# Kernel optimization log

Hardware: AMD Instinct MI355X
Metric: run time of the kernel (lower is better)

## Reference

```python
import jax, jax.numpy as jnp
import numpy as np

BITS = 4
GROUP_SIZE = 128
INF, OUTF, TOKENS = 4096, 11008, 256


def setup_inputs() -> dict:
    key = jax.random.key(0)
    k1, k2, k3, k4, k5 = jax.random.split(key, 5)
    n_groups = INF // GROUP_SIZE  # 32
    x = jax.random.normal(k1, (TOKENS, INF), dtype=jnp.float32)
    qweight = jax.random.randint(k2, (INF // 32 * BITS, OUTF), 0, 2**31 - 1, dtype=jnp.int32)
    qzeros = jax.random.randint(k3, (n_groups, OUTF // 32 * BITS), 0, 2**31 - 1, dtype=jnp.int32)
    scales = jax.random.uniform(k4, (n_groups, OUTF), dtype=jnp.float32, minval=1e-3, maxval=2e-2)
    bias = jax.random.normal(k5, (OUTF,), dtype=jnp.float32)
    return {"x": x, "qweight": qweight, "qzeros": qzeros, "scales": scales, "bias": bias}


def _dequantize(qweight, qzeros, scales):
    """Unpack int4 nibbles and build the fp32 weight [infeatures, outfeatures]."""
    shifts = jnp.arange(0, 32, BITS, dtype=jnp.int32)  # [8]
    mask = (1 << BITS) - 1
    out_f = qweight.shape[1]
    # qweight row packs 8 consecutive in-features -> [K, O] int in [0, 15]
    w = ((qweight[:, None, :] >> shifts[None, :, None]) & mask).reshape(-1, out_f)
    # qzeros col packs 8 consecutive out-features; stored as (zero - 1)
    n_groups = qzeros.shape[0]
    z = (((qzeros[:, :, None] >> shifts[None, None, :]) & mask) + 1).reshape(n_groups, out_f)
    g_idx = jnp.arange(w.shape[0], dtype=jnp.int32) // GROUP_SIZE  # [K]
    return (w - z[g_idx]).astype(jnp.float32) * scales[g_idx]


def reference(x, qweight, qzeros, scales, bias):
    W = _dequantize(qweight, qzeros, scales)  # [infeatures, outfeatures]
    return x @ W + bias  # [tokens, outfeatures]
```

## Files before the change

### kernel.cpp

```cpp
#include <hip/hip_runtime.h>
#include <stdint.h>

#define TOKENS  256
#define INF     4096
#define OUTF    11008
#define NGROUPS 32
#define KSPLIT  2
#define PHK     128
#define NPH     ((INF / KSPLIT) / PHK)
#define NTH     256

typedef __attribute__((ext_vector_type(2))) _Float16 f16x2;
typedef __attribute__((ext_vector_type(8))) _Float16 f16x8;
typedef __attribute__((ext_vector_type(2))) __fp16   pkh2;
typedef __attribute__((ext_vector_type(4))) float    f32x4;

union U32H2 { uint32_t u; f16x2 h; };
union H8    { f16x2 h2[4]; f16x8 h8; };
union PK    { pkh2 p; f16x2 h; };

__device__ __forceinline__ void gl2lds16(const void* g, void* l) {
    __builtin_amdgcn_global_load_lds(
        (const __attribute__((address_space(1))) uint32_t*)g,
        (__attribute__((address_space(3))) uint32_t*)l, 16, 0, 0);
}

__global__ __launch_bounds__(NTH)
void prep(const float* __restrict__ x, _Float16* __restrict__ x16,
          const float* __restrict__ bias, float* __restrict__ out) {
    const int b = blockIdx.x;
    if (b < 512) {
        const int t   = b * NTH + threadIdx.x;
        const int row = t >> 9;
        const int c   = t & 511;
        const float* p = x + (size_t)row * INF + c * 8;
        f32x4 v0 = *(const f32x4*)p;
        f32x4 v1 = *(const f32x4*)(p + 4);
        H8 o; PK k0, k1, k2, k3;
        k0.p = __builtin_amdgcn_cvt_pkrtz(v0[0], v1[0]);
        k1.p = __builtin_amdgcn_cvt_pkrtz(v0[1], v1[1]);
        k2.p = __builtin_amdgcn_cvt_pkrtz(v0[2], v1[2]);
        k3.p = __builtin_amdgcn_cvt_pkrtz(v0[3], v1[3]);
        o.h2[0] = k0.h; o.h2[1] = k1.h; o.h2[2] = k2.h; o.h2[3] = k3.h;
        *(f16x8*)(x16 + (size_t)row * INF + c * 8) = o.h8;
    } else {
        const int t = (b - 512) * NTH + threadIdx.x;
        const int c = t % (OUTF / 4);
        const int r = t / (OUTF / 4);
        const f32x4 bv = ((const f32x4*)bias)[c];
        ((f32x4*)out)[(size_t)r * (OUTF / 4) + c] = bv;
    }
}

__global__ __launch_bounds__(NTH, 3)
void qlin_main(const _Float16* __restrict__ x16,
               const uint32_t* __restrict__ qweight,
               const uint32_t* __restrict__ qzeros,
               const float* __restrict__ scales,
               float* __restrict__ out)
{
    __shared__ alignas(16) _Float16 As[2][64 * PHK];

    const int tid = threadIdx.x;

    const int d  = blockIdx.x;
    const int cx = d & 7, kk = d >> 3;
    int strip, memb;
    if (kk < 80) { strip = cx * 10 + (kk >> 3); memb = kk & 7; }
    else         { const int t2 = ((kk - 80) << 3) | cx; strip = 80 + (t2 >> 3); memb = t2 & 7; }
    const int bx = strip;
    const int by = memb >> 1;
    const int ks = memb & 1;

    const int lane = tid & 63;
    const int quad = lane >> 4;
    const int l16  = lane & 15;
    const int wv   = tid >> 6;

    const int rowoff = tid >> 4;
    const int chk    = tid & 15;
    const int row0   = by * 64;
    const uint32_t aoff = (uint32_t)((row0 + rowoff) * (INF * 2)
                                     + ks * (INF / KSPLIT) * 2
                                     + ((chk ^ rowoff) & 15) * 16);
    const char* x16b = (const char*)x16;
    _Float16* ldsW = &As[0][0];
    const int ldsSlotBase = wv * 512;

    const int col0 = bx * 128 + wv * 32 + l16;
    const int col1 = col0 + 16;
    const int bOff0 = quad * OUTF + col0;
    const int bOff1 = quad * OUTF + col1;
    const int zsh   = (col0 & 7) * 4;
    const int qrow0 = ks * (INF / KSPLIT / 8);
    const int g0    = ks * (NGROUPS / KSPLIT);

    f32x4 acc[4][2];
#pragma unroll
    for (int mi = 0; mi < 4; ++mi)
#pragma unroll
        for (int nf = 0; nf < 2; ++nf)
            acc[mi][nf] = f32x4{0.f, 0.f, 0.f, 0.f};

    uint32_t Breg[2][8];
    float    sS[2][2];
    uint32_t qZ[2][2];

#pragma unroll
    for (int r = 0; r < 4; ++r)
        gl2lds16(x16b + aoff + r * 131072, ldsW + r * 2048 + ldsSlotBase);
    __builtin_amdgcn_sched_barrier(0);
    {
        sS[0][0] = scales[g0 * OUTF + col0];
        sS[0][1] = scales[g0 * OUTF + col1];
        qZ[0][0] = qzeros[g0 * (OUTF / 8) + (col0 >> 3)];
        qZ[0][1] = qzeros[g0 * (OUTF / 8) + (col1 >> 3)];
        const uint32_t* qp = qweight + (size_t)qrow0 * OUTF;
#pragma unroll
        for (int s = 0; s < 4; ++s) {
            Breg[0][2 * s + 0] = qp[(size_t)(s * 4) * OUTF + bOff0];
            Breg[0][2 * s + 1] = qp[(size_t)(s * 4) * OUTF + bOff1];
        }
    }

#define PHASE_BODY(PAR, P, DO_PREFETCH)                                          \
    {                                                                            \
        __builtin_amdgcn_sched_barrier(0);                                       \
        asm volatile("s_waitcnt vmcnt(8)" ::: "memory");                         \
        __builtin_amdgcn_s_barrier();                                            \
        __builtin_amdgcn_sched_barrier(0);                                       \
        if (DO_PREFETCH) {                                                       \
            const int pn = (P) + 1;                                              \
            const uint32_t pb = (uint32_t)(pn * (PHK * 2));                      \
            _Float16* ldsN = ldsW + (1 - (PAR)) * 8192;                          \
            _Pragma("unroll")                                                    \
            for (int r = 0; r < 4; ++r)                                          \
                gl2lds16(x16b + aoff + r * 131072 + pb,                          \
                         ldsN + r * 2048 + ldsSlotBase);                         \
            __builtin_amdgcn_sched_barrier(0);           \
            const int gn = g0 + pn;                                              \
            sS[1 - (PAR)][0] = scales[gn * OUTF + col0];                         \
            sS[1 - (PAR)][1] = scales[gn * OUTF + col1];                         \
            qZ[1 - (PAR)][0] = qzeros[gn * (OUTF / 8) + (col0 >> 3)];            \
            qZ[1 - (PAR)][1] = qzeros[gn * (OUTF / 8) + (col1 >> 3)];            \
            const uint32_t* qpb = qweight + (size_t)(qrow0 + pn * 16) * OUTF;    \
            _Pragma("unroll")                                                    \
            for (int s = 0; s < 4; ++s) {                                        \
                Breg[1 - (PAR)][2 * s + 0] = qpb[(size_t)(s * 4) * OUTF + bOff0];\
                Breg[1 - (PAR)][2 * s + 1] = qpb[(size_t)(s * 4) * OUTF + bOff1];\
            }                                                                    \
        }                                                                        \
        f16x2 hs2[2], hz2[2];                                                    \
        _Pragma("unroll")                                                        \
        for (int nf = 0; nf < 2; ++nf) {                                         \
            const float s = sS[PAR][nf];                                         \
            const int   z = (int)((qZ[PAR][nf] >> zsh) & 15u) + 1025;            \
            const _Float16 hs = (_Float16)s;                                     \
            const _Float16 hz = (_Float16)(-(float)z);                           \
            hs2[nf] = f16x2{hs, hs};                                             \
            hz2[nf] = f16x2{hz, hz};                                             \
        }                                                                        \
        const _Float16* buf = ldsW + (PAR) * 8192;                               \
        _Pragma("unroll")                                                        \
        for (int s = 0; s < 4; ++s) {                                            \
            f16x8 af[4];                                                         \
            _Pragma("unroll")                                                    \
            for (int mi = 0; mi < 4; ++mi) {                                     \
                const int m  = mi * 16 + l16;                                    \
                const int sc = ((s * 4 + quad) ^ l16) & 15;                      \
                af[mi] = *(const f16x8*)(buf + m * PHK + sc * 8);                \
            }                                                                    \
            _Pragma("unroll")                                                    \
            for (int nf = 0; nf < 2; ++nf) {                                     \
                const uint32_t q = Breg[PAR][2 * s + nf];                        \
                H8 b;                                                            \
                _Pragma("unroll")                                                \
                for (int j = 0; j < 4; ++j) {                                    \
                    U32H2 u;                                                     \
                    u.u = ((q >> (4 * j)) & 0x000F000Fu) | 0x64006400u;          \
                    b.h2[j] = (u.h + hz2[nf]) * hs2[nf];                         \
                }                                                                \
                __builtin_amdgcn_s_setprio(1);                                   \
                _Pragma("unroll")                                                \
                for (int mi = 0; mi < 4; ++mi)                                   \
                    acc[mi][nf] = __builtin_amdgcn_mfma_f32_16x16x32_f16(        \
                        af[mi], b.h8, acc[mi][nf], 0, 0, 0);                     \
                __builtin_amdgcn_s_setprio(0);                                   \
            }                                                                    \
        }                                                                        \
    }

#pragma unroll 1
    for (int pp = 0; pp < NPH / 2; ++pp) {
        PHASE_BODY(0, 2 * pp, true)
        PHASE_BODY(1, 2 * pp + 1, (pp < NPH / 2 - 1))
    }
#undef PHASE_BODY

#pragma unroll
    for (int nf = 0; nf < 2; ++nf) {
        const int col = (nf == 0) ? col0 : col1;
#pragma unroll
        for (int mi = 0; mi < 4; ++mi) {
            const int r0 = by * 64 + mi * 16 + quad * 4;
#pragma unroll
            for (int rg = 0; rg < 4; ++rg)
                unsafeAtomicAdd(&out[(size_t)(r0 + rg) * OUTF + col],
                                acc[mi][nf][rg]);
        }
    }
}

__global__ __launch_bounds__(NTH, 2)
void qlin_fb(const float* __restrict__ x,
             const uint32_t* __restrict__ qweight,
             const uint32_t* __restrict__ qzeros,
             const float* __restrict__ scales,
             const float* __restrict__ bias,
             float* __restrict__ out)
{
    __shared__ alignas(16) _Float16 Asb[64][40];
    __shared__ alignas(16) _Float16 Bsb[128][40];
    const int tid = threadIdx.x;
    const int bx = blockIdx.x, by = blockIdx.y;
    const int am = tid >> 2, ar = tid & 3;
    const float* xrow = x + (size_t)(by * 64 + am) * INF + ar * 8;
    const int bc = tid & 127, br = tid >> 7;
    const int bn = bx * 128 + bc;
    const int bswz = (bc >> 3) & 3;
    const int lane = tid & 63, quad = lane >> 4, l16 = lane & 15;
    const int wv = tid >> 6, wm = wv >> 1, wn = wv & 1;
    f32x4 acc[2][4];
#pragma unroll
    for (int i = 0; i < 2; ++i)
#pragma unroll
        for (int j = 0; j < 4; ++j) acc[i][j] = f32x4{0.f, 0.f, 0.f, 0.f};
    f32x4 pa0 = *(const f32x4*)(xrow + 0);
    f32x4 pa1 = *(const f32x4*)(xrow + 4);
    uint32_t pq0 = qweight[(size_t)br * OUTF + bn];
    uint32_t pq1 = qweight[(size_t)(br + 2) * OUTF + bn];
    for (int g = 0; g < NGROUPS; ++g) {
        const float s = scales[g * OUTF + bn];
        const uint32_t qzv = qzeros[g * (OUTF / 8) + (bn >> 3)];
        const int z = (int)((qzv >> (4 * (bn & 7))) & 15u) + 1;
        const _Float16 hs = (_Float16)s;
        const _Float16 hz = (_Float16)(-(float)(1024 + z));
        const f16x2 hs2 = {hs, hs}, hz2 = {hz, hz};
#pragma unroll
        for (int t4 = 0; t4 < 4; ++t4) {
            const int it = (g << 2) + t4;
            { H8 ah; PK p0, p1, p2, p3;
              p0.p = __builtin_amdgcn_cvt_pkrtz(pa0[0], pa1[0]);
              p1.p = __builtin_amdgcn_cvt_pkrtz(pa0[1], pa1[1]);
              p2.p = __builtin_amdgcn_cvt_pkrtz(pa0[2], pa1[2]);
              p3.p = __builtin_amdgcn_cvt_pkrtz(pa0[3], pa1[3]);
              ah.h2[0] = p0.h; ah.h2[1] = p1.h; ah.h2[2] = p2.h; ah.h2[3] = p3.h;
              *(f16x8*)&Asb[am][ar * 8] = ah.h8; }
            { const uint32_t qq[2] = {pq0, pq1};
#pragma unroll
              for (int rr = 0; rr < 2; ++rr) {
                  const int r = br + rr * 2; H8 bh;
#pragma unroll
                  for (int jp = 0; jp < 4; ++jp) {
                      U32H2 u; u.u = ((qq[rr] >> (4 * jp)) & 0x000F000Fu) | 0x64006400u;
                      bh.h2[jp] = (u.h + hz2) * hs2;
                  }
                  *(f16x8*)&Bsb[bc][(r ^ bswz) * 8] = bh.h8;
              } }
            __syncthreads();
            const int itn = (it < 127) ? it + 1 : 127;
            pa0 = *(const f32x4*)(xrow + itn * 32);
            pa1 = *(const f32x4*)(xrow + itn * 32 + 4);
            pq0 = qweight[(size_t)(itn * 4 + br) * OUTF + bn];
            pq1 = qweight[(size_t)(itn * 4 + br + 2) * OUTF + bn];
            f16x8 af[2], bf[4];
#pragma unroll
            for (int mi = 0; mi < 2; ++mi)
                af[mi] = *(const f16x8*)&Asb[wm * 32 + mi * 16 + l16][quad * 8];
#pragma unroll
            for (int ni = 0; ni < 4; ++ni) {
                const int c = wn * 64 + ni * 16 + l16;
                bf[ni] = *(const f16x8*)&Bsb[c][(quad ^ ((c >> 3) & 3)) * 8];
            }
#pragma unroll
            for (int mi = 0; mi < 2; ++mi)
#pragma unroll
                for (int ni = 0; ni < 4; ++ni)
                    acc[mi][ni] = __builtin_amdgcn_mfma_f32_16x16x32_f16(
                        af[mi], bf[ni], acc[mi][ni], 0, 0, 0);
            __syncthreads();
        }
    }
#pragma unroll
    for (int ni = 0; ni < 4; ++ni) {
        const int col = bx * 128 + wn * 64 + ni * 16 + l16;
        const float bv = bias[col];
#pragma unroll
        for (int mi = 0; mi < 2; ++mi) {
            const int row0 = by * 64 + wm * 32 + mi * 16 + quad * 4;
#pragma unroll
            for (int rg = 0; rg < 4; ++rg)
                out[(size_t)(row0 + rg) * OUTF + col] = acc[mi][ni][rg] + bv;
        }
    }
}

extern "C" void kernel_launch(void* const* d_in, const int* in_sizes, int n_in,
                              void* d_out, int out_size, void* d_ws, size_t ws_size,
                              hipStream_t stream) {
    const float*    xx = (const float*)d_in[0];
    const uint32_t* qw = (const uint32_t*)d_in[1];
    const uint32_t* qz = (const uint32_t*)d_in[2];
    const float*    sc = (const float*)d_in[3];
    const float*    bs = (const float*)d_in[4];
    float* out = (float*)d_out;

    const size_t x16_bytes = (size_t)TOKENS * INF * sizeof(_Float16);
    if (ws_size >= x16_bytes) {
        _Float16* x16 = (_Float16*)d_ws;
        prep<<<512 + (TOKENS * OUTF / 4) / NTH, NTH, 0, stream>>>(xx, x16, bs, out);
        qlin_main<<<(OUTF / 128) * (TOKENS / 64) * KSPLIT, NTH, 0, stream>>>(
            x16, qw, qz, sc, out);
    } else {
        dim3 grid(OUTF / 128, TOKENS / 64);
        qlin_fb<<<grid, NTH, 0, stream>>>(xx, qw, qz, sc, bs, out);
    }
}
```

Baseline: 122.2 us.

## Load activation fragments directly from global memory instead of LDS staging

Removes the LDS double buffer for the fp16 activations, along with the global_load_lds prefetch, the vmcnt wait and the block-wide barrier in each phase. Each wave now reads its A fragments straight from global memory (through the cache) just before the MFMAs. This drops the barrier synchronisation and the LDS traffic, but the four waves now each fetch the same A tile redundantly, and those loads are no longer prefetched a phase ahead, so their latency is exposed.

```diff
diff --git a/kernel.cpp b/kernel.cpp
--- a/kernel.cpp
+++ b/kernel.cpp
@@ -18,12 +18,6 @@
 union U32H2 { uint32_t u; f16x2 h; };
 union H8    { f16x2 h2[4]; f16x8 h8; };
 union PK    { pkh2 p; f16x2 h; };
-
-__device__ __forceinline__ void gl2lds16(const void* g, void* l) {
-    __builtin_amdgcn_global_load_lds(
-        (const __attribute__((address_space(1))) uint32_t*)g,
-        (__attribute__((address_space(3))) uint32_t*)l, 16, 0, 0);
-}
 
 __global__ __launch_bounds__(NTH)
 void prep(const float* __restrict__ x, _Float16* __restrict__ x16,
@@ -59,8 +53,6 @@
                const float* __restrict__ scales,
                float* __restrict__ out)
 {
-    __shared__ alignas(16) _Float16 As[2][64 * PHK];
-
     const int tid = threadIdx.x;
 
     const int d  = blockIdx.x;
@@ -77,15 +69,8 @@
     const int l16  = lane & 15;
     const int wv   = tid >> 6;
 
-    const int rowoff = tid >> 4;
-    const int chk    = tid & 15;
-    const int row0   = by * 64;
-    const uint32_t aoff = (uint32_t)((row0 + rowoff) * (INF * 2)
-                                     + ks * (INF / KSPLIT) * 2
-                                     + ((chk ^ rowoff) & 15) * 16);
-    const char* x16b = (const char*)x16;
-    _Float16* ldsW = &As[0][0];
-    const int ldsSlotBase = wv * 512;
+    const _Float16* aBase = x16 + (size_t)(by * 64 + l16) * INF
+                                + ks * (INF / KSPLIT) + quad * 8;
 
     const int col0 = bx * 128 + wv * 32 + l16;
     const int col1 = col0 + 16;
@@ -106,10 +91,6 @@
     float    sS[2][2];
     uint32_t qZ[2][2];
 
-#pragma unroll
-    for (int r = 0; r < 4; ++r)
-        gl2lds16(x16b + aoff + r * 131072, ldsW + r * 2048 + ldsSlotBase);
-    __builtin_amdgcn_sched_barrier(0);
     {
         sS[0][0] = scales[g0 * OUTF + col0];
         sS[0][1] = scales[g0 * OUTF + col1];
@@ -125,19 +106,8 @@
 
 #define PHASE_BODY(PAR, P, DO_PREFETCH)                                          \
     {                                                                            \
-        __builtin_amdgcn_sched_barrier(0);                                       \
-        asm volatile("s_waitcnt vmcnt(8)" ::: "memory");                         \
-        __builtin_amdgcn_s_barrier();                                            \
-        __builtin_amdgcn_sched_barrier(0);                                       \
         if (DO_PREFETCH) {                                                       \
             const int pn = (P) + 1;                                              \
-            const uint32_t pb = (uint32_t)(pn * (PHK * 2));                      \
-            _Float16* ldsN = ldsW + (1 - (PAR)) * 8192;                          \
-            _Pragma("unroll")                                                    \
-            for (int r = 0; r < 4; ++r)                                          \
-                gl2lds16(x16b + aoff + r * 131072 + pb,                          \
-                         ldsN + r * 2048 + ldsSlotBase);                         \
-            __builtin_amdgcn_sched_barrier(0);           \
             const int gn = g0 + pn;                                              \
             sS[1 - (PAR)][0] = scales[gn * OUTF + col0];                         \
             sS[1 - (PAR)][1] = scales[gn * OUTF + col1];                         \
@@ -160,16 +130,13 @@
             hs2[nf] = f16x2{hs, hs};                                             \
             hz2[nf] = f16x2{hz, hz};                                             \
         }                                                                        \
-        const _Float16* buf = ldsW + (PAR) * 8192;                               \
+        const _Float16* aP = aBase + (P) * PHK;                                  \
         _Pragma("unroll")                                                        \
         for (int s = 0; s < 4; ++s) {                                            \
             f16x8 af[4];                                                         \
             _Pragma("unroll")                                                    \
-            for (int mi = 0; mi < 4; ++mi) {                                     \
-                const int m  = mi * 16 + l16;                                    \
-                const int sc = ((s * 4 + quad) ^ l16) & 15;                      \
-                af[mi] = *(const f16x8*)(buf + m * PHK + sc * 8);                \
-            }                                                                    \
+            for (int mi = 0; mi < 4; ++mi)                                       \
+                af[mi] = *(const f16x8*)(aP + (size_t)mi * (16 * INF) + s * 32); \
             _Pragma("unroll")                                                    \
             for (int nf = 0; nf < 2; ++nf) {                                     \
                 const uint32_t q = Breg[PAR][2 * s + nf];                        \
```

New measurement: 173.7 us. 1.42x slower.

## Widen output tile to 256 columns per block to double A-tile reuse

Applied to the files above, without the earlier changes.

Each block now covers 256 output columns, with each wave holding 4 N-fragments, so every A tile staged in LDS feeds twice as many MFMAs. The grid halves to 344 blocks and the block-to-tile mapping is changed to a simple strided interleave. Occupancy drops to 2 blocks per CU because the accumulator and prefetched weight registers double, and the vmcnt wait is raised to match the larger number of in-flight weight loads. The trade is more reuse and less staging of A through LDS, against fewer resident waves and only 344 blocks to spread across the CUs.

```diff
diff --git a/kernel.cpp b/kernel.cpp
--- a/kernel.cpp
+++ b/kernel.cpp
@@ -9,6 +9,7 @@
 #define PHK     128
 #define NPH     ((INF / KSPLIT) / PHK)
 #define NTH     256
+#define BN      256
 
 typedef __attribute__((ext_vector_type(2))) _Float16 f16x2;
 typedef __attribute__((ext_vector_type(8))) _Float16 f16x8;
@@ -52,7 +53,7 @@
     }
 }
 
-__global__ __launch_bounds__(NTH, 3)
+__global__ __launch_bounds__(NTH, 2)
 void qlin_main(const _Float16* __restrict__ x16,
                const uint32_t* __restrict__ qweight,
                const uint32_t* __restrict__ qzeros,
@@ -63,12 +64,10 @@
 
     const int tid = threadIdx.x;
 
-    const int d  = blockIdx.x;
-    const int cx = d & 7, kk = d >> 3;
-    int strip, memb;
-    if (kk < 80) { strip = cx * 10 + (kk >> 3); memb = kk & 7; }
-    else         { const int t2 = ((kk - 80) << 3) | cx; strip = 80 + (t2 >> 3); memb = t2 & 7; }
-    const int bx = strip;
+    const int d   = blockIdx.x;
+    const int lin = (d & 7) * 43 + (d >> 3);
+    const int bx   = lin >> 3;
+    const int memb = lin & 7;
     const int by = memb >> 1;
     const int ks = memb & 1;
 
@@ -87,72 +86,70 @@
     _Float16* ldsW = &As[0][0];
     const int ldsSlotBase = wv * 512;
 
-    const int col0 = bx * 128 + wv * 32 + l16;
-    const int col1 = col0 + 16;
-    const int bOff0 = quad * OUTF + col0;
-    const int bOff1 = quad * OUTF + col1;
-    const int zsh   = (col0 & 7) * 4;
+    int colN[4], bOffN[4], zOffN[4];
+#pragma unroll
+    for (int nf = 0; nf < 4; ++nf) {
+        colN[nf]  = bx * BN + wv * 64 + nf * 16 + l16;
+        bOffN[nf] = quad * OUTF + colN[nf];
+        zOffN[nf] = colN[nf] >> 3;
+    }
+    const int zsh   = (l16 & 7) * 4;
     const int qrow0 = ks * (INF / KSPLIT / 8);
     const int g0    = ks * (NGROUPS / KSPLIT);
 
-    f32x4 acc[4][2];
+    f32x4 acc[4][4];
 #pragma unroll
     for (int mi = 0; mi < 4; ++mi)
 #pragma unroll
-        for (int nf = 0; nf < 2; ++nf)
+        for (int nf = 0; nf < 4; ++nf)
             acc[mi][nf] = f32x4{0.f, 0.f, 0.f, 0.f};
 
-    uint32_t Breg[2][8];
-    float    sS[2][2];
-    uint32_t qZ[2][2];
+    uint32_t Breg[2][16];
+    float    sS[2][4];
+    uint32_t qZ[2][4];
+
+#define LOAD_B(SLOT, PN)                                                         \
+    {                                                                            \
+        const int gn_ = g0 + (PN);                                               \
+        _Pragma("unroll")                                                        \
+        for (int nf = 0; nf < 4; ++nf) {                                         \
+            sS[SLOT][nf] = scales[gn_ * OUTF + colN[nf]];                        \
+            qZ[SLOT][nf] = qzeros[gn_ * (OUTF / 8) + zOffN[nf]];                 \
+        }                                                                        \
+        const uint32_t* qpb_ = qweight + (size_t)(qrow0 + (PN) * 16) * OUTF;     \
+        _Pragma("unroll")                                                        \
+        for (int s_ = 0; s_ < 4; ++s_)                                           \
+            _Pragma("unroll")                                                    \
+            for (int nf = 0; nf < 4; ++nf)                                       \
+                Breg[SLOT][s_ * 4 + nf] =                                        \
+                    qpb_[(size_t)(s_ * 4) * OUTF + bOffN[nf]];                   \
+    }
 
 #pragma unroll
     for (int r = 0; r < 4; ++r)
         gl2lds16(x16b + aoff + r * 131072, ldsW + r * 2048 + ldsSlotBase);
     __builtin_amdgcn_sched_barrier(0);
-    {
-        sS[0][0] = scales[g0 * OUTF + col0];
-        sS[0][1] = scales[g0 * OUTF + col1];
-        qZ[0][0] = qzeros[g0 * (OUTF / 8) + (col0 >> 3)];
-        qZ[0][1] = qzeros[g0 * (OUTF / 8) + (col1 >> 3)];
-        const uint32_t* qp = qweight + (size_t)qrow0 * OUTF;
-#pragma unroll
-        for (int s = 0; s < 4; ++s) {
-            Breg[0][2 * s + 0] = qp[(size_t)(s * 4) * OUTF + bOff0];
-            Breg[0][2 * s + 1] = qp[(size_t)(s * 4) * OUTF + bOff1];
-        }
-    }
-
-#define PHASE_BODY(PAR, P, DO_PREFETCH)                                          \
+    LOAD_B(0, 0)
+
+#define PHASE_BODY(PAR, P, DO_PRE)                                               \
     {                                                                            \
         __builtin_amdgcn_sched_barrier(0);                                       \
-        asm volatile("s_waitcnt vmcnt(8)" ::: "memory");                         \
+        asm volatile("s_waitcnt vmcnt(16)" ::: "memory");                        \
         __builtin_amdgcn_s_barrier();                                            \
         __builtin_amdgcn_sched_barrier(0);                                       \
-        if (DO_PREFETCH) {                                                       \
-            const int pn = (P) + 1;                                              \
-            const uint32_t pb = (uint32_t)(pn * (PHK * 2));                      \
+        if (DO_PRE) {                                                            \
+            const uint32_t pb = (uint32_t)(((P) + 1) * (PHK * 2));               \
             _Float16* ldsN = ldsW + (1 - (PAR)) * 8192;                          \
             _Pragma("unroll")                                                    \
             for (int r = 0; r < 4; ++r)                                          \
                 gl2lds16(x16b + aoff + r * 131072 + pb,                          \
                          ldsN + r * 2048 + ldsSlotBase);                         \
-            __builtin_amdgcn_sched_barrier(0);           \
-            const int gn = g0 + pn;                                              \
-            sS[1 - (PAR)][0] = scales[gn * OUTF + col0];                         \
-            sS[1 - (PAR)][1] = scales[gn * OUTF + col1];                         \
-            qZ[1 - (PAR)][0] = qzeros[gn * (OUTF / 8) + (col0 >> 3)];            \
-            qZ[1 - (PAR)][1] = qzeros[gn * (OUTF / 8) + (col1 >> 3)];            \
-            const uint32_t* qpb = qweight + (size_t)(qrow0 + pn * 16) * OUTF;    \
-            _Pragma("unroll")                                                    \
-            for (int s = 0; s < 4; ++s) {                                        \
-                Breg[1 - (PAR)][2 * s + 0] = qpb[(size_t)(s * 4) * OUTF + bOff0];\
-                Breg[1 - (PAR)][2 * s + 1] = qpb[(size_t)(s * 4) * OUTF + bOff1];\
-            }                                                                    \
+            __builtin_amdgcn_sched_barrier(0);        \
+            LOAD_B(1 - (PAR), (P) + 1)                                           \
         }                                                                        \
-        f16x2 hs2[2], hz2[2];                                                    \
+        f16x2 hs2[4], hz2[4];                                                    \
         _Pragma("unroll")                                                        \
-        for (int nf = 0; nf < 2; ++nf) {                                         \
+        for (int nf = 0; nf < 4; ++nf) {                                         \
             const float s = sS[PAR][nf];                                         \
             const int   z = (int)((qZ[PAR][nf] >> zsh) & 15u) + 1025;            \
             const _Float16 hs = (_Float16)s;                                     \
@@ -171,8 +168,8 @@
                 af[mi] = *(const f16x8*)(buf + m * PHK + sc * 8);                \
             }                                                                    \
             _Pragma("unroll")                                                    \
-            for (int nf = 0; nf < 2; ++nf) {                                     \
-                const uint32_t q = Breg[PAR][2 * s + nf];                        \
+            for (int nf = 0; nf < 4; ++nf) {                                     \
+                const uint32_t q = Breg[PAR][s * 4 + nf];                        \
                 H8 b;                                                            \
                 _Pragma("unroll")                                                \
                 for (int j = 0; j < 4; ++j) {                                    \
@@ -196,10 +193,11 @@
         PHASE_BODY(1, 2 * pp + 1, (pp < NPH / 2 - 1))
     }
 #undef PHASE_BODY
-
-#pragma unroll
-    for (int nf = 0; nf < 2; ++nf) {
-        const int col = (nf == 0) ? col0 : col1;
+#undef LOAD_B
+
+#pragma unroll
+    for (int nf = 0; nf < 4; ++nf) {
+        const int col = colN[nf];
 #pragma unroll
         for (int mi = 0; mi < 4; ++mi) {
             const int r0 = by * 64 + mi * 16 + quad * 4;
@@ -319,7 +317,7 @@
     if (ws_size >= x16_bytes) {
         _Float16* x16 = (_Float16*)d_ws;
         prep<<<512 + (TOKENS * OUTF / 4) / NTH, NTH, 0, stream>>>(xx, x16, bs, out);
-        qlin_main<<<(OUTF / 128) * (TOKENS / 64) * KSPLIT, NTH, 0, stream>>>(
+        qlin_main<<<(OUTF / BN) * (TOKENS / 64) * KSPLIT, NTH, 0, stream>>>(
             x16, qw, qz, sc, out);
     } else {
         dim3 grid(OUTF / 128, TOKENS / 64);
```

Result: slower. 132.1 us (+8.1%).
